# Optimization experiments

Measured on AMD Instinct MI355X. Metric: run time of the kernel, lower is better.

The kernel has to match this reference:

```python
import jax, jax.numpy as jnp
import numpy as np

B, S, H, NH = 2, 2048, 1024, 16
HD = H // NH  # 64
EPS = 1e-5


def setup_inputs() -> dict:
    key = jax.random.key(0)
    ks = jax.random.split(key, 4)
    return {
        "hidden_states": jax.random.normal(ks[0], (B, S, H), dtype=jnp.float32),
        "W_attn": jax.random.normal(ks[1], (H, 3 * H), dtype=jnp.float32) * (1.0 / np.sqrt(H)),
        "b_attn": jnp.zeros((3 * H,), dtype=jnp.float32),
        "W_proj": jax.random.normal(ks[2], (H, H), dtype=jnp.float32) * (1.0 / np.sqrt(H)),
        "b_proj": jnp.zeros((H,), dtype=jnp.float32),
        "q_gamma": jnp.ones((HD,), dtype=jnp.float32),
        "q_beta": jnp.zeros((HD,), dtype=jnp.float32),
        "k_gamma": jnp.ones((HD,), dtype=jnp.float32),
        "k_beta": jnp.zeros((HD,), dtype=jnp.float32),
    }


def _layernorm(x, gamma, beta):
    mu = jnp.mean(x, axis=-1, keepdims=True)
    var = jnp.mean(jnp.square(x - mu), axis=-1, keepdims=True)
    return (x - mu) * jax.lax.rsqrt(var + EPS) * gamma + beta


def reference(hidden_states, W_attn, b_attn, W_proj, b_proj, q_gamma, q_beta, k_gamma, k_beta):
    b, s, h = hidden_states.shape
    qkv = hidden_states @ W_attn + b_attn  # [B,S,3H]
    q, k, v = jnp.split(qkv, 3, axis=-1)
    # [B,S,H] -> [B,NH,S,HD]
    def to_heads(t):
        return t.reshape(b, s, NH, HD).transpose(0, 2, 1, 3)
    q, k, v = to_heads(q), to_heads(k), to_heads(v)
    # QK LayerNorm over head_dim
    q = _layernorm(q, q_gamma, q_beta)
    k = _layernorm(k, k_gamma, k_beta)
    scale = HD ** (-0.5)
    scores = jnp.einsum("bhqd,bhkd->bhqk", q, k) * scale
    causal = jnp.tril(jnp.ones((s, s), dtype=bool))
    mask_value = jnp.finfo(scores.dtype).min
    scores = jnp.where(causal, scores, mask_value)
    attn = jax.nn.softmax(scores.astype(jnp.float32), axis=-1).astype(q.dtype)
    out = jnp.einsum("bhqk,bhkd->bhqd", attn, v)
    out = out.transpose(0, 2, 1, 3).reshape(b, s, h)
    out = out @ W_proj + b_proj
    return out
```

## Files before the change

kernel.cpp:

```cpp
#include <hip/hip_runtime.h>
#include <hip/hip_bf16.h>

typedef __bf16 bf16x8 __attribute__((ext_vector_type(8)));
typedef float f32x4 __attribute__((ext_vector_type(4)));

#define EPS 1e-5f
#define QSCALE 0.18033688011112042f

__device__ __forceinline__ unsigned short f2bf(float f) {
  union { float f; unsigned int i; } c; c.f = f;
  unsigned int r = c.i + 0x7FFFu + ((c.i >> 16) & 1u);
  return (unsigned short)(r >> 16);
}

__global__ __launch_bounds__(256) void transpose_f32_bf16(
    const float* __restrict__ in, unsigned short* __restrict__ out,
    int R, int C)
{
  __shared__ __align__(16) unsigned short S[64 * 72];
  const int t = threadIdx.x;
  const int r = t >> 2, c4 = (t & 3) * 16;
  const int rt0 = blockIdx.y * 64, ct0 = blockIdx.x * 64;

  {
    long base = (long)(rt0 + r) * C + ct0 + c4;
    float4 a = *(const float4*)&in[base];
    float4 b = *(const float4*)&in[base + 4];
    float4 c = *(const float4*)&in[base + 8];
    float4 d = *(const float4*)&in[base + 12];
    unsigned short v[16] = {f2bf(a.x), f2bf(a.y), f2bf(a.z), f2bf(a.w),
                            f2bf(b.x), f2bf(b.y), f2bf(b.z), f2bf(b.w),
                            f2bf(c.x), f2bf(c.y), f2bf(c.z), f2bf(c.w),
                            f2bf(d.x), f2bf(d.y), f2bf(d.z), f2bf(d.w)};
    *(uint4*)&S[r * 72 + c4]     = *(uint4*)&v[0];
    *(uint4*)&S[r * 72 + c4 + 8] = *(uint4*)&v[8];
  }
  __syncthreads();

  unsigned short tmp[16];
#pragma unroll
  for (int j = 0; j < 16; j++) tmp[j] = S[(c4 + j) * 72 + r];
  *(uint4*)&out[(long)(ct0 + r) * R + rt0 + c4]     = *(uint4*)&tmp[0];
  *(uint4*)&out[(long)(ct0 + r) * R + rt0 + c4 + 8] = *(uint4*)&tmp[8];
}

__global__ __launch_bounds__(256) void convert_f32_bf16(
    const float* __restrict__ in, unsigned short* __restrict__ out)
{
  long i = ((long)blockIdx.x * 256 + threadIdx.x) * 16;
  float4 a = *(const float4*)&in[i];
  float4 b = *(const float4*)&in[i + 4];
  float4 c = *(const float4*)&in[i + 8];
  float4 d = *(const float4*)&in[i + 12];
  unsigned short v[16] = {f2bf(a.x), f2bf(a.y), f2bf(a.z), f2bf(a.w),
                          f2bf(b.x), f2bf(b.y), f2bf(b.z), f2bf(b.w),
                          f2bf(c.x), f2bf(c.y), f2bf(c.z), f2bf(c.w),
                          f2bf(d.x), f2bf(d.y), f2bf(d.z), f2bf(d.w)};
  *(uint4*)&out[i]     = *(uint4*)&v[0];
  *(uint4*)&out[i + 8] = *(uint4*)&v[8];
}

__global__ __launch_bounds__(256) void qkv_ln_kernel(
    const float* __restrict__ Xf,
    const unsigned short* __restrict__ Xbf, int use_xbf,
    const unsigned short* __restrict__ WT,
    const float* __restrict__ bias,
    const float* __restrict__ qg, const float* __restrict__ qb,
    const float* __restrict__ kg, const float* __restrict__ kb,
    unsigned short* __restrict__ Qws, unsigned short* __restrict__ Kws,
    unsigned short* __restrict__ Vws)
{
  __shared__ __align__(16) unsigned short As[2][128 * 32];
  __shared__ __align__(16) unsigned short Bs[2][128 * 32];

  const int tid = threadIdx.x;
  const int w = tid >> 6, lane = tid & 63, quad = lane >> 4, l15 = lane & 15;
  const int mh = w & 1, nh = w >> 1;
  const int n0 = blockIdx.x * 128, m0 = blockIdx.y * 128;

  f32x4 acc[4][4];
#pragma unroll
  for (int i = 0; i < 4; i++)
#pragma unroll
    for (int j = 0; j < 4; j++) acc[i][j] = (f32x4){0.f, 0.f, 0.f, 0.f};

  const int sr2 = tid >> 1, sh2 = (tid & 1) * 16;

  if (use_xbf) {
    long xo = (long)(m0 + sr2) * 1024 + sh2;
    *(uint4*)&As[0][sr2 * 32 + sh2]     = *(const uint4*)&Xbf[xo];
    *(uint4*)&As[0][sr2 * 32 + sh2 + 8] = *(const uint4*)&Xbf[xo + 8];
  } else {
    long xo = (long)(m0 + sr2) * 1024 + sh2;
    float4 a0 = *(const float4*)&Xf[xo];
    float4 a1 = *(const float4*)&Xf[xo + 4];
    float4 a2 = *(const float4*)&Xf[xo + 8];
    float4 a3 = *(const float4*)&Xf[xo + 12];
    unsigned short v[16] = {f2bf(a0.x), f2bf(a0.y), f2bf(a0.z), f2bf(a0.w),
                            f2bf(a1.x), f2bf(a1.y), f2bf(a1.z), f2bf(a1.w),
                            f2bf(a2.x), f2bf(a2.y), f2bf(a2.z), f2bf(a2.w),
                            f2bf(a3.x), f2bf(a3.y), f2bf(a3.z), f2bf(a3.w)};
    *(uint4*)&As[0][sr2 * 32 + sh2]     = *(uint4*)&v[0];
    *(uint4*)&As[0][sr2 * 32 + sh2 + 8] = *(uint4*)&v[8];
  }
  {
    long wo = (long)(n0 + sr2) * 1024 + sh2;
    *(uint4*)&Bs[0][sr2 * 32 + sh2]     = *(const uint4*)&WT[wo];
    *(uint4*)&Bs[0][sr2 * 32 + sh2 + 8] = *(const uint4*)&WT[wo + 8];
  }
  __syncthreads();

  int buf = 0;
  for (int kt = 0; kt < 1024; kt += 32) {
    const int nbuf = buf ^ 1;
    const bool pf = (kt + 32) < 1024;
    uint4 xv0, xv1, wv0, wv1;
    float4 a0, a1, a2, a3;
    if (pf) {
      if (use_xbf) {
        long xo = (long)(m0 + sr2) * 1024 + kt + 32 + sh2;
        xv0 = *(const uint4*)&Xbf[xo];
        xv1 = *(const uint4*)&Xbf[xo + 8];
      } else {
        long xo = (long)(m0 + sr2) * 1024 + kt + 32 + sh2;
        a0 = *(const float4*)&Xf[xo];
        a1 = *(const float4*)&Xf[xo + 4];
        a2 = *(const float4*)&Xf[xo + 8];
        a3 = *(const float4*)&Xf[xo + 12];
      }
      long wo = (long)(n0 + sr2) * 1024 + kt + 32 + sh2;
      wv0 = *(const uint4*)&WT[wo];
      wv1 = *(const uint4*)&WT[wo + 8];
    }

    bf16x8 af[4], bfr[4];
#pragma unroll
    for (int mq = 0; mq < 4; mq++)
      af[mq] = *(const bf16x8*)&As[buf][(mh * 64 + mq * 16 + l15) * 32 + quad * 8];
#pragma unroll
    for (int nq = 0; nq < 4; nq++)
      bfr[nq] = *(const bf16x8*)&Bs[buf][(nh * 64 + nq * 16 + l15) * 32 + quad * 8];
#pragma unroll
    for (int mq = 0; mq < 4; mq++)
#pragma unroll
      for (int nq = 0; nq < 4; nq++)
        acc[mq][nq] = __builtin_amdgcn_mfma_f32_16x16x32_bf16(af[mq], bfr[nq], acc[mq][nq], 0, 0, 0);

    if (pf) {
      if (use_xbf) {
        *(uint4*)&As[nbuf][sr2 * 32 + sh2]     = xv0;
        *(uint4*)&As[nbuf][sr2 * 32 + sh2 + 8] = xv1;
      } else {
        unsigned short v[16] = {f2bf(a0.x), f2bf(a0.y), f2bf(a0.z), f2bf(a0.w),
                                f2bf(a1.x), f2bf(a1.y), f2bf(a1.z), f2bf(a1.w),
                                f2bf(a2.x), f2bf(a2.y), f2bf(a2.z), f2bf(a2.w),
                                f2bf(a3.x), f2bf(a3.y), f2bf(a3.z), f2bf(a3.w)};
        *(uint4*)&As[nbuf][sr2 * 32 + sh2]     = *(uint4*)&v[0];
        *(uint4*)&As[nbuf][sr2 * 32 + sh2 + 8] = *(uint4*)&v[8];
      }
      *(uint4*)&Bs[nbuf][sr2 * 32 + sh2]     = wv0;
      *(uint4*)&Bs[nbuf][sr2 * 32 + sh2 + 8] = wv1;
    }
    __syncthreads();
    buf = nbuf;
  }

#pragma unroll
  for (int nq = 0; nq < 4; nq++) {
    float bv = bias[n0 + nh * 64 + nq * 16 + l15];
#pragma unroll
    for (int mq = 0; mq < 4; mq++)
#pragma unroll
      for (int rr = 0; rr < 4; rr++) acc[mq][nq][rr] += bv;
  }

  const int g = (n0 >> 6) + nh;
  const bool isQ = g < 16, isK = (g >= 16) && (g < 32);

  if (isQ || isK) {
    float gv[4], bev[4];
#pragma unroll
    for (int nq = 0; nq < 4; nq++) {
      int d = nq * 16 + l15;
      gv[nq]  = isQ ? qg[d] : kg[d];
      bev[nq] = isQ ? qb[d] : kb[d];
      if (isQ) { gv[nq] *= QSCALE; bev[nq] *= QSCALE; }
    }
#pragma unroll
    for (int mq = 0; mq < 4; mq++)
#pragma unroll
      for (int rr = 0; rr < 4; rr++) {
        float s  = acc[mq][0][rr] + acc[mq][1][rr] + acc[mq][2][rr] + acc[mq][3][rr];
        float s2 = acc[mq][0][rr]*acc[mq][0][rr] + acc[mq][1][rr]*acc[mq][1][rr]
                 + acc[mq][2][rr]*acc[mq][2][rr] + acc[mq][3][rr]*acc[mq][3][rr];
#pragma unroll
        for (int off = 1; off < 16; off <<= 1) {
          s  += __shfl_xor(s,  off, 64);
          s2 += __shfl_xor(s2, off, 64);
        }
        float mu   = s * (1.0f / 64.0f);
        float var  = fmaxf(s2 * (1.0f / 64.0f) - mu * mu, 0.f);
        float rstd = rsqrtf(var + EPS);
#pragma unroll
        for (int nq = 0; nq < 4; nq++)
          acc[mq][nq][rr] = (acc[mq][nq][rr] - mu) * rstd * gv[nq] + bev[nq];
      }
  }

  unsigned short* dst; int head;
  if (isQ)      { dst = Qws; head = g; }
  else if (isK) { dst = Kws; head = g - 16; }
  else          { dst = Vws; head = g - 32; }

#pragma unroll
  for (int mq = 0; mq < 4; mq++)
#pragma unroll
    for (int rr = 0; rr < 4; rr++) {
      int m = m0 + mh * 64 + mq * 16 + quad * 4 + rr;
      int b = m >> 11, s = m & 2047;
      long base = ((long)((b * 16 + head) * 2048 + s)) * 64;
#pragma unroll
      for (int nq = 0; nq < 4; nq++)
        dst[base + nq * 16 + l15] = f2bf(acc[mq][nq][rr]);
    }
}

__global__ __launch_bounds__(256) void attn_kernel(
    unsigned short* __restrict__ Qws,
    const unsigned short* __restrict__ Kws,
    const unsigned short* __restrict__ Vws)
{
  __shared__ __align__(16) unsigned short Ks[2][64 * 72];
  __shared__ __align__(16) unsigned short VTs[2][64 * 72];
  __shared__ __align__(16) unsigned short Ps[64 * 64];

  const int tid = threadIdx.x;
  const int w = tid >> 6, lane = tid & 63, quad = lane >> 4, l15 = lane & 15;
  const int bh = blockIdx.y;
  const int qt = ((bh >> 3) & 1) ? blockIdx.x : (31 - blockIdx.x);
  const int qbase = qt * 64;
  const long bhoff = (long)bh * 2048 * 64;
  const int jmax = qt + 1;

  const int sr = tid >> 2, sc = (tid & 3) * 16;
  const int vrow = lane, vc = w * 16;

  *(uint4*)&Ps[sr * 64 + sc]     = *(const uint4*)&Qws[bhoff + (qbase + sr) * 64 + sc];
  *(uint4*)&Ps[sr * 64 + sc + 8] = *(const uint4*)&Qws[bhoff + (qbase + sr) * 64 + sc + 8];
  *(uint4*)&Ks[0][sr * 72 + sc]     = *(const uint4*)&Kws[bhoff + sr * 64 + sc];
  *(uint4*)&Ks[0][sr * 72 + sc + 8] = *(const uint4*)&Kws[bhoff + sr * 64 + sc + 8];
  {
    uint4 v0 = *(const uint4*)&Vws[bhoff + vrow * 64 + vc];
    uint4 v1 = *(const uint4*)&Vws[bhoff + vrow * 64 + vc + 8];
    const unsigned short* vv = (const unsigned short*)&v0;
#pragma unroll
    for (int t = 0; t < 8; t++) VTs[0][(vc + t) * 72 + vrow] = vv[t];
    vv = (const unsigned short*)&v1;
#pragma unroll
    for (int t = 0; t < 8; t++) VTs[0][(vc + 8 + t) * 72 + vrow] = vv[t];
  }
  __syncthreads();

  const bf16x8 qf0 = *(const bf16x8*)&Ps[(w * 16 + l15) * 64 + quad * 8];
  const bf16x8 qf1 = *(const bf16x8*)&Ps[(w * 16 + l15) * 64 + 32 + quad * 8];
  __syncthreads();

  bf16x8 ones;
  {
    union { unsigned short u[8]; bf16x8 v; } c;
#pragma unroll
    for (int i = 0; i < 8; i++) c.u[i] = 0x3F80u;
    ones = c.v;
  }

  f32x4 o[4], osum;
#pragma unroll
  for (int i = 0; i < 4; i++) o[i] = (f32x4){0.f, 0.f, 0.f, 0.f};
  osum = (f32x4){0.f, 0.f, 0.f, 0.f};

  const int sw = ((l15 >> 2) & 3) << 4;
  const int pc0 = (quad * 8) ^ sw;
  const int pc1 = (32 + quad * 8) ^ sw;

  int buf = 0;
  for (int j = 0; j < jmax; j++) {
    const int nbuf = buf ^ 1;
    const int kb = j * 64;
    const bool pf = (j + 1) < jmax;
    uint4 pk0, pk1, pv0, pv1;
    if (pf) {
      const int kb1 = kb + 64;
      pk0 = *(const uint4*)&Kws[bhoff + (kb1 + sr) * 64 + sc];
      pk1 = *(const uint4*)&Kws[bhoff + (kb1 + sr) * 64 + sc + 8];
      pv0 = *(const uint4*)&Vws[bhoff + (kb1 + vrow) * 64 + vc];
      pv1 = *(const uint4*)&Vws[bhoff + (kb1 + vrow) * 64 + vc + 8];
    }

    f32x4 sacc[4];
#pragma unroll
    for (int i = 0; i < 4; i++) sacc[i] = (f32x4){0.f, 0.f, 0.f, 0.f};
#pragma unroll
    for (int nt = 0; nt < 4; nt++) {
      bf16x8 kf0 = *(const bf16x8*)&Ks[buf][(nt * 16 + l15) * 72 + quad * 8];
      bf16x8 kf1 = *(const bf16x8*)&Ks[buf][(nt * 16 + l15) * 72 + 32 + quad * 8];
      sacc[nt] = __builtin_amdgcn_mfma_f32_16x16x32_bf16(qf0, kf0, sacc[nt], 0, 0, 0);
      sacc[nt] = __builtin_amdgcn_mfma_f32_16x16x32_bf16(qf1, kf1, sacc[nt], 0, 0, 0);
    }

    if (pf) {
      *(uint4*)&Ks[nbuf][sr * 72 + sc]     = pk0;
      *(uint4*)&Ks[nbuf][sr * 72 + sc + 8] = pk1;
      const unsigned short* vv = (const unsigned short*)&pv0;
#pragma unroll
      for (int t = 0; t < 8; t++) VTs[nbuf][(vc + t) * 72 + vrow] = vv[t];
      vv = (const unsigned short*)&pv1;
#pragma unroll
      for (int t = 0; t < 8; t++) VTs[nbuf][(vc + 8 + t) * 72 + vrow] = vv[t];
    }

    const bool domask = (j == qt);
#pragma unroll
    for (int nt = 0; nt < 4; nt++)
#pragma unroll
      for (int rr = 0; rr < 4; rr++) {
        float p = exp2f(sacc[nt][rr]);
        if (domask) {
          int kcol = kb + nt * 16 + l15;
          int qrow = qbase + w * 16 + quad * 4 + rr;
          if (kcol > qrow) p = 0.f;
        }
        sacc[nt][rr] = p;
      }

#pragma unroll
    for (int rr = 0; rr < 4; rr++)
#pragma unroll
      for (int nt = 0; nt < 4; nt++)
        Ps[(w * 16 + quad * 4 + rr) * 64 + (((nt ^ quad) & 3) * 16 + l15)]
            = f2bf(sacc[nt][rr]);

    bf16x8 pfr0 = *(const bf16x8*)&Ps[(w * 16 + l15) * 64 + pc0];
    bf16x8 pfr1 = *(const bf16x8*)&Ps[(w * 16 + l15) * 64 + pc1];

    osum = __builtin_amdgcn_mfma_f32_16x16x32_bf16(pfr0, ones, osum, 0, 0, 0);
    osum = __builtin_amdgcn_mfma_f32_16x16x32_bf16(pfr1, ones, osum, 0, 0, 0);
#pragma unroll
    for (int dt = 0; dt < 4; dt++) {
      bf16x8 vf0 = *(const bf16x8*)&VTs[buf][(dt * 16 + l15) * 72 + quad * 8];
      bf16x8 vf1 = *(const bf16x8*)&VTs[buf][(dt * 16 + l15) * 72 + 32 + quad * 8];
      o[dt] = __builtin_amdgcn_mfma_f32_16x16x32_bf16(pfr0, vf0, o[dt], 0, 0, 0);
      o[dt] = __builtin_amdgcn_mfma_f32_16x16x32_bf16(pfr1, vf1, o[dt], 0, 0, 0);
    }
    __syncthreads();
    buf = nbuf;
  }

#pragma unroll
  for (int rr = 0; rr < 4; rr++) {
    float inv = 1.0f / osum[rr];
    int row = qbase + w * 16 + quad * 4 + rr;
    long base = bhoff + (long)row * 64;
#pragma unroll
    for (int dt = 0; dt < 4; dt++)
      Qws[base + dt * 16 + l15] = f2bf(o[dt][rr] * inv);
  }
}

__global__ __launch_bounds__(256) void proj_kernel(
    const unsigned short* __restrict__ AQ,
    const unsigned short* __restrict__ WT,
    const float* __restrict__ bias,
    float* __restrict__ Out)
{
  __shared__ __align__(16) unsigned short As[2][128 * 32];
  __shared__ __align__(16) unsigned short Bs[2][128 * 32];

  const int tid = threadIdx.x;
  const int w = tid >> 6, lane = tid & 63, quad = lane >> 4, l15 = lane & 15;
  const int mh = w & 1, nh = w >> 1;
  const int n0 = blockIdx.x * 128, m0 = blockIdx.y * 128;

  f32x4 acc[4][4];
#pragma unroll
  for (int i = 0; i < 4; i++)
#pragma unroll
    for (int j = 0; j < 4; j++) acc[i][j] = (f32x4){0.f, 0.f, 0.f, 0.f};

  const int sr2 = tid >> 1, sh2 = (tid & 1) * 16;
  const int m = m0 + sr2, b = m >> 11, s = m & 2047;

  {
    const int h = sh2 >> 6, d = sh2 & 63;
    long ao = ((long)((b * 16 + h) * 2048 + s)) * 64 + d;
    *(uint4*)&As[0][sr2 * 32 + sh2]     = *(const uint4*)&AQ[ao];
    *(uint4*)&As[0][sr2 * 32 + sh2 + 8] = *(const uint4*)&AQ[ao + 8];
    long wo = (long)(n0 + sr2) * 1024 + sh2;
    *(uint4*)&Bs[0][sr2 * 32 + sh2]     = *(const uint4*)&WT[wo];
    *(uint4*)&Bs[0][sr2 * 32 + sh2 + 8] = *(const uint4*)&WT[wo + 8];
  }
  __syncthreads();

  int buf = 0;
  for (int kt = 0; kt < 1024; kt += 32) {
    const int nbuf = buf ^ 1;
    const bool pf = (kt + 32) < 1024;
    uint4 av0, av1, wv0, wv1;
    if (pf) {
      const int k = kt + 32 + sh2, h = k >> 6, d = k & 63;
      long ao = ((long)((b * 16 + h) * 2048 + s)) * 64 + d;
      av0 = *(const uint4*)&AQ[ao];
      av1 = *(const uint4*)&AQ[ao + 8];
      long wo = (long)(n0 + sr2) * 1024 + kt + 32 + sh2;
      wv0 = *(const uint4*)&WT[wo];
      wv1 = *(const uint4*)&WT[wo + 8];
    }

    bf16x8 af[4], bfr[4];
#pragma unroll
    for (int mq = 0; mq < 4; mq++)
      af[mq] = *(const bf16x8*)&As[buf][(mh * 64 + mq * 16 + l15) * 32 + quad * 8];
#pragma unroll
    for (int nq = 0; nq < 4; nq++)
      bfr[nq] = *(const bf16x8*)&Bs[buf][(nh * 64 + nq * 16 + l15) * 32 + quad * 8];
#pragma unroll
    for (int mq = 0; mq < 4; mq++)
#pragma unroll
      for (int nq = 0; nq < 4; nq++)
        acc[mq][nq] = __builtin_amdgcn_mfma_f32_16x16x32_bf16(af[mq], bfr[nq], acc[mq][nq], 0, 0, 0);

    if (pf) {
      *(uint4*)&As[nbuf][sr2 * 32 + sh2]     = av0;
      *(uint4*)&As[nbuf][sr2 * 32 + sh2 + 8] = av1;
      *(uint4*)&Bs[nbuf][sr2 * 32 + sh2]     = wv0;
      *(uint4*)&Bs[nbuf][sr2 * 32 + sh2 + 8] = wv1;
    }
    __syncthreads();
    buf = nbuf;
  }

#pragma unroll
  for (int nq = 0; nq < 4; nq++) {
    int n = n0 + nh * 64 + nq * 16 + l15;
    float bv = bias[n];
#pragma unroll
    for (int mq = 0; mq < 4; mq++)
#pragma unroll
      for (int rr = 0; rr < 4; rr++) {
        int mm = m0 + mh * 64 + mq * 16 + quad * 4 + rr;
        Out[(long)mm * 1024 + n] = acc[mq][nq][rr] + bv;
      }
  }
}

extern "C" void kernel_launch(void* const* d_in, const int* in_sizes, int n_in,
                              void* d_out, int out_size, void* d_ws, size_t ws_size,
                              hipStream_t stream) {
  const float* X  = (const float*)d_in[0];
  const float* Wa = (const float*)d_in[1];
  const float* ba = (const float*)d_in[2];
  const float* Wp = (const float*)d_in[3];
  const float* bp = (const float*)d_in[4];
  const float* qg = (const float*)d_in[5];
  const float* qb = (const float*)d_in[6];
  const float* kg = (const float*)d_in[7];
  const float* kb = (const float*)d_in[8];

  const long per = 2L * 16 * 2048 * 64;
  unsigned short* ws  = (unsigned short*)d_ws;
  unsigned short* Qws = ws;
  unsigned short* Kws = Qws + per;
  unsigned short* Vws = Kws + per;

  const bool big = ws_size >= (size_t)(5L * per * 2);
  unsigned short *Xbf, *WaT, *WpT;
  if (big) {
    Xbf = Vws + per;
    WaT = Xbf + per;
    WpT = WaT + 3072L * 1024;
  } else {
    Xbf = Qws;
    WaT = Vws + per;
    WpT = WaT + 3072L * 1024;
  }

  transpose_f32_bf16<<<dim3(48, 16), 256, 0, stream>>>(Wa, WaT, 1024, 3072);
  transpose_f32_bf16<<<dim3(16, 16), 256, 0, stream>>>(Wp, WpT, 1024, 1024);
  if (big) convert_f32_bf16<<<1024, 256, 0, stream>>>(X, Xbf);
  qkv_ln_kernel<<<dim3(24, 32), 256, 0, stream>>>(X, Xbf, big ? 1 : 0, WaT, ba,
                                                  qg, qb, kg, kb, Qws, Kws, Vws);
  attn_kernel<<<dim3(32, 32), 256, 0, stream>>>(Qws, Kws, Vws);
  proj_kernel<<<dim3(8, 32), 256, 0, stream>>>(Qws, WpT, bp, (float*)d_out);
}
```

Before: 243.4 us.

## Compute V directly in transposed layout via separate GEMM kernel; single-buffer attention LDS

Moves the V projection out of the QKV kernel into a new GEMM, W_v^T times X^T, that writes V already transposed per head ([B,NH,HD,S]). The attention kernel can then load V^T tiles with vector copies instead of scattering 16 scalar LDS writes per thread. The attention K and V^T shared buffers are cut from double to single buffering, with an extra barrier pair around each refill. Launch bounds are raised to ask for 6 blocks per CU, trading load/compute overlap inside a block for occupancy. This adds a kernel launch, and the V GEMM writes scattered 2-byte stores along S.

After: 222.1 us. 1.1x faster.

```diff
diff --git a/kernel.cpp b/kernel.cpp
--- a/kernel.cpp
+++ b/kernel.cpp
@@ -67,8 +67,7 @@
     const float* __restrict__ bias,
     const float* __restrict__ qg, const float* __restrict__ qb,
     const float* __restrict__ kg, const float* __restrict__ kb,
-    unsigned short* __restrict__ Qws, unsigned short* __restrict__ Kws,
-    unsigned short* __restrict__ Vws)
+    unsigned short* __restrict__ Qws, unsigned short* __restrict__ Kws)
 {
   __shared__ __align__(16) unsigned short As[2][128 * 32];
   __shared__ __align__(16) unsigned short Bs[2][128 * 32];
@@ -175,9 +174,9 @@
   }
 
   const int g = (n0 >> 6) + nh;
-  const bool isQ = g < 16, isK = (g >= 16) && (g < 32);
-
-  if (isQ || isK) {
+  const bool isQ = g < 16;
+
+  {
     float gv[4], bev[4];
 #pragma unroll
     for (int nq = 0; nq < 4; nq++) {
@@ -207,10 +206,8 @@
       }
   }
 
-  unsigned short* dst; int head;
-  if (isQ)      { dst = Qws; head = g; }
-  else if (isK) { dst = Kws; head = g - 16; }
-  else          { dst = Vws; head = g - 32; }
+  unsigned short* dst = isQ ? Qws : Kws;
+  const int head = isQ ? g : g - 16;
 
 #pragma unroll
   for (int mq = 0; mq < 4; mq++)
@@ -225,13 +222,130 @@
     }
 }
 
-__global__ __launch_bounds__(256) void attn_kernel(
+__global__ __launch_bounds__(256) void vt_kernel(
+    const float* __restrict__ Xf,
+    const unsigned short* __restrict__ Xbf, int use_xbf,
+    const unsigned short* __restrict__ WvT,
+    const float* __restrict__ bias,
+    unsigned short* __restrict__ Vt)
+{
+  __shared__ __align__(16) unsigned short As[2][128 * 32];
+  __shared__ __align__(16) unsigned short Bs[2][128 * 32];
+
+  const int tid = threadIdx.x;
+  const int w = tid >> 6, lane = tid & 63, quad = lane >> 4, l15 = lane & 15;
+  const int mh = w & 1, nh = w >> 1;
+  const int n0 = blockIdx.x * 128, m0 = blockIdx.y * 128, bz = blockIdx.z;
+  const long xrow0 = (long)bz * 2048;
+
+  f32x4 acc[4][4];
+#pragma unroll
+  for (int i = 0; i < 4; i++)
+#pragma unroll
+    for (int j = 0; j < 4; j++) acc[i][j] = (f32x4){0.f, 0.f, 0.f, 0.f};
+
+  const int sr2 = tid >> 1, sh2 = (tid & 1) * 16;
+
+  {
+    long wo = (long)(m0 + sr2) * 1024 + sh2;
+    *(uint4*)&As[0][sr2 * 32 + sh2]     = *(const uint4*)&WvT[wo];
+    *(uint4*)&As[0][sr2 * 32 + sh2 + 8] = *(const uint4*)&WvT[wo + 8];
+  }
+  if (use_xbf) {
+    long xo = (xrow0 + n0 + sr2) * 1024 + sh2;
+    *(uint4*)&Bs[0][sr2 * 32 + sh2]     = *(const uint4*)&Xbf[xo];
+    *(uint4*)&Bs[0][sr2 * 32 + sh2 + 8] = *(const uint4*)&Xbf[xo + 8];
+  } else {
+    long xo = (xrow0 + n0 + sr2) * 1024 + sh2;
+    float4 a0 = *(const float4*)&Xf[xo];
+    float4 a1 = *(const float4*)&Xf[xo + 4];
+    float4 a2 = *(const float4*)&Xf[xo + 8];
+    float4 a3 = *(const float4*)&Xf[xo + 12];
+    unsigned short v[16] = {f2bf(a0.x), f2bf(a0.y), f2bf(a0.z), f2bf(a0.w),
+                            f2bf(a1.x), f2bf(a1.y), f2bf(a1.z), f2bf(a1.w),
+                            f2bf(a2.x), f2bf(a2.y), f2bf(a2.z), f2bf(a2.w),
+                            f2bf(a3.x), f2bf(a3.y), f2bf(a3.z), f2bf(a3.w)};
+    *(uint4*)&Bs[0][sr2 * 32 + sh2]     = *(uint4*)&v[0];
+    *(uint4*)&Bs[0][sr2 * 32 + sh2 + 8] = *(uint4*)&v[8];
+  }
+  __syncthreads();
+
+  int buf = 0;
+  for (int kt = 0; kt < 1024; kt += 32) {
+    const int nbuf = buf ^ 1;
+    const bool pf = (kt + 32) < 1024;
+    uint4 wv0, wv1, xv0, xv1;
+    float4 a0, a1, a2, a3;
+    if (pf) {
+      long wo = (long)(m0 + sr2) * 1024 + kt + 32 + sh2;
+      wv0 = *(const uint4*)&WvT[wo];
+      wv1 = *(const uint4*)&WvT[wo + 8];
+      long xo = (xrow0 + n0 + sr2) * 1024 + kt + 32 + sh2;
+      if (use_xbf) {
+        xv0 = *(const uint4*)&Xbf[xo];
+        xv1 = *(const uint4*)&Xbf[xo + 8];
+      } else {
+        a0 = *(const float4*)&Xf[xo];
+        a1 = *(const float4*)&Xf[xo + 4];
+        a2 = *(const float4*)&Xf[xo + 8];
+        a3 = *(const float4*)&Xf[xo + 12];
+      }
+    }
+
+    bf16x8 af[4], bfr[4];
+#pragma unroll
+    for (int mq = 0; mq < 4; mq++)
+      af[mq] = *(const bf16x8*)&As[buf][(mh * 64 + mq * 16 + l15) * 32 + quad * 8];
+#pragma unroll
+    for (int nq = 0; nq < 4; nq++)
+      bfr[nq] = *(const bf16x8*)&Bs[buf][(nh * 64 + nq * 16 + l15) * 32 + quad * 8];
+#pragma unroll
+    for (int mq = 0; mq < 4; mq++)
+#pragma unroll
+      for (int nq = 0; nq < 4; nq++)
+        acc[mq][nq] = __builtin_amdgcn_mfma_f32_16x16x32_bf16(af[mq], bfr[nq], acc[mq][nq], 0, 0, 0);
+
+    if (pf) {
+      *(uint4*)&As[nbuf][sr2 * 32 + sh2]     = wv0;
+      *(uint4*)&As[nbuf][sr2 * 32 + sh2 + 8] = wv1;
+      if (use_xbf) {
+        *(uint4*)&Bs[nbuf][sr2 * 32 + sh2]     = xv0;
+        *(uint4*)&Bs[nbuf][sr2 * 32 + sh2 + 8] = xv1;
+      } else {
+        unsigned short v[16] = {f2bf(a0.x), f2bf(a0.y), f2bf(a0.z), f2bf(a0.w),
+                                f2bf(a1.x), f2bf(a1.y), f2bf(a1.z), f2bf(a1.w),
+                                f2bf(a2.x), f2bf(a2.y), f2bf(a2.z), f2bf(a2.w),
+                                f2bf(a3.x), f2bf(a3.y), f2bf(a3.z), f2bf(a3.w)};
+        *(uint4*)&Bs[nbuf][sr2 * 32 + sh2]     = *(uint4*)&v[0];
+        *(uint4*)&Bs[nbuf][sr2 * 32 + sh2 + 8] = *(uint4*)&v[8];
+      }
+    }
+    __syncthreads();
+    buf = nbuf;
+  }
+
+  const long outb = (long)bz * 2097152;
+#pragma unroll
+  for (int mq = 0; mq < 4; mq++)
+#pragma unroll
+    for (int rr = 0; rr < 4; rr++) {
+      int m = m0 + mh * 64 + mq * 16 + quad * 4 + rr;
+      float bv = bias[2048 + m];
+#pragma unroll
+      for (int nq = 0; nq < 4; nq++) {
+        int n = n0 + nh * 64 + nq * 16 + l15;
+        Vt[outb + (long)m * 2048 + n] = f2bf(acc[mq][nq][rr] + bv);
+      }
+    }
+}
+
+__global__ __launch_bounds__(256, 6) void attn_kernel(
     unsigned short* __restrict__ Qws,
     const unsigned short* __restrict__ Kws,
-    const unsigned short* __restrict__ Vws)
+    const unsigned short* __restrict__ Vt)
 {
-  __shared__ __align__(16) unsigned short Ks[2][64 * 72];
-  __shared__ __align__(16) unsigned short VTs[2][64 * 72];
+  __shared__ __align__(16) unsigned short Ks[64 * 72];
+  __shared__ __align__(16) unsigned short VTs[64 * 72];
   __shared__ __align__(16) unsigned short Ps[64 * 64];
 
   const int tid = threadIdx.x;
@@ -240,30 +354,21 @@
   const int qt = ((bh >> 3) & 1) ? blockIdx.x : (31 - blockIdx.x);
   const int qbase = qt * 64;
   const long bhoff = (long)bh * 2048 * 64;
+  const long bhv   = (long)bh * 131072;
   const int jmax = qt + 1;
 
   const int sr = tid >> 2, sc = (tid & 3) * 16;
-  const int vrow = lane, vc = w * 16;
 
   *(uint4*)&Ps[sr * 64 + sc]     = *(const uint4*)&Qws[bhoff + (qbase + sr) * 64 + sc];
   *(uint4*)&Ps[sr * 64 + sc + 8] = *(const uint4*)&Qws[bhoff + (qbase + sr) * 64 + sc + 8];
-  *(uint4*)&Ks[0][sr * 72 + sc]     = *(const uint4*)&Kws[bhoff + sr * 64 + sc];
-  *(uint4*)&Ks[0][sr * 72 + sc + 8] = *(const uint4*)&Kws[bhoff + sr * 64 + sc + 8];
-  {
-    uint4 v0 = *(const uint4*)&Vws[bhoff + vrow * 64 + vc];
-    uint4 v1 = *(const uint4*)&Vws[bhoff + vrow * 64 + vc + 8];
-    const unsigned short* vv = (const unsigned short*)&v0;
-#pragma unroll
-    for (int t = 0; t < 8; t++) VTs[0][(vc + t) * 72 + vrow] = vv[t];
-    vv = (const unsigned short*)&v1;
-#pragma unroll
-    for (int t = 0; t < 8; t++) VTs[0][(vc + 8 + t) * 72 + vrow] = vv[t];
-  }
+  *(uint4*)&Ks[sr * 72 + sc]      = *(const uint4*)&Kws[bhoff + sr * 64 + sc];
+  *(uint4*)&Ks[sr * 72 + sc + 8]  = *(const uint4*)&Kws[bhoff + sr * 64 + sc + 8];
+  *(uint4*)&VTs[sr * 72 + sc]     = *(const uint4*)&Vt[bhv + sr * 2048 + sc];
+  *(uint4*)&VTs[sr * 72 + sc + 8] = *(const uint4*)&Vt[bhv + sr * 2048 + sc + 8];
   __syncthreads();
 
   const bf16x8 qf0 = *(const bf16x8*)&Ps[(w * 16 + l15) * 64 + quad * 8];
   const bf16x8 qf1 = *(const bf16x8*)&Ps[(w * 16 + l15) * 64 + 32 + quad * 8];
-  __syncthreads();
 
   bf16x8 ones;
   {
@@ -282,9 +387,7 @@
   const int pc0 = (quad * 8) ^ sw;
   const int pc1 = (32 + quad * 8) ^ sw;
 
-  int buf = 0;
   for (int j = 0; j < jmax; j++) {
-    const int nbuf = buf ^ 1;
     const int kb = j * 64;
     const bool pf = (j + 1) < jmax;
     uint4 pk0, pk1, pv0, pv1;
@@ -292,8 +395,8 @@
       const int kb1 = kb + 64;
       pk0 = *(const uint4*)&Kws[bhoff + (kb1 + sr) * 64 + sc];
       pk1 = *(const uint4*)&Kws[bhoff + (kb1 + sr) * 64 + sc + 8];
-      pv0 = *(const uint4*)&Vws[bhoff + (kb1 + vrow) * 64 + vc];
-      pv1 = *(const uint4*)&Vws[bhoff + (kb1 + vrow) * 64 + vc + 8];
+      pv0 = *(const uint4*)&Vt[bhv + sr * 2048 + kb1 + sc];
+      pv1 = *(const uint4*)&Vt[bhv + sr * 2048 + kb1 + sc + 8];
     }
 
     f32x4 sacc[4];
@@ -301,21 +404,10 @@
     for (int i = 0; i < 4; i++) sacc[i] = (f32x4){0.f, 0.f, 0.f, 0.f};
 #pragma unroll
     for (int nt = 0; nt < 4; nt++) {
-      bf16x8 kf0 = *(const bf16x8*)&Ks[buf][(nt * 16 + l15) * 72 + quad * 8];
-      bf16x8 kf1 = *(const bf16x8*)&Ks[buf][(nt * 16 + l15) * 72 + 32 + quad * 8];
+      bf16x8 kf0 = *(const bf16x8*)&Ks[(nt * 16 + l15) * 72 + quad * 8];
+      bf16x8 kf1 = *(const bf16x8*)&Ks[(nt * 16 + l15) * 72 + 32 + quad * 8];
       sacc[nt] = __builtin_amdgcn_mfma_f32_16x16x32_bf16(qf0, kf0, sacc[nt], 0, 0, 0);
       sacc[nt] = __builtin_amdgcn_mfma_f32_16x16x32_bf16(qf1, kf1, sacc[nt], 0, 0, 0);
-    }
-
-    if (pf) {
-      *(uint4*)&Ks[nbuf][sr * 72 + sc]     = pk0;
-      *(uint4*)&Ks[nbuf][sr * 72 + sc + 8] = pk1;
-      const unsigned short* vv = (const unsigned short*)&pv0;
-#pragma unroll
-      for (int t = 0; t < 8; t++) VTs[nbuf][(vc + t) * 72 + vrow] = vv[t];
-      vv = (const unsigned short*)&pv1;
-#pragma unroll
-      for (int t = 0; t < 8; t++) VTs[nbuf][(vc + 8 + t) * 72 + vrow] = vv[t];
     }
 
     const bool domask = (j == qt);
@@ -346,13 +438,20 @@
     osum = __builtin_amdgcn_mfma_f32_16x16x32_bf16(pfr1, ones, osum, 0, 0, 0);
 #pragma unroll
     for (int dt = 0; dt < 4; dt++) {
-      bf16x8 vf0 = *(const bf16x8*)&VTs[buf][(dt * 16 + l15) * 72 + quad * 8];
-      bf16x8 vf1 = *(const bf16x8*)&VTs[buf][(dt * 16 + l15) * 72 + 32 + quad * 8];
+      bf16x8 vf0 = *(const bf16x8*)&VTs[(dt * 16 + l15) * 72 + quad * 8];
+      bf16x8 vf1 = *(const bf16x8*)&VTs[(dt * 16 + l15) * 72 + 32 + quad * 8];
       o[dt] = __builtin_amdgcn_mfma_f32_16x16x32_bf16(pfr0, vf0, o[dt], 0, 0, 0);
       o[dt] = __builtin_amdgcn_mfma_f32_16x16x32_bf16(pfr1, vf1, o[dt], 0, 0, 0);
     }
-    __syncthreads();
-    buf = nbuf;
+
+    if (pf) {
+      __syncthreads();
+      *(uint4*)&Ks[sr * 72 + sc]      = pk0;
+      *(uint4*)&Ks[sr * 72 + sc + 8]  = pk1;
+      *(uint4*)&VTs[sr * 72 + sc]     = pv0;
+      *(uint4*)&VTs[sr * 72 + sc + 8] = pv1;
+      __syncthreads();
+    }
   }
 
 #pragma unroll
@@ -469,25 +568,27 @@
   unsigned short* ws  = (unsigned short*)d_ws;
   unsigned short* Qws = ws;
   unsigned short* Kws = Qws + per;
-  unsigned short* Vws = Kws + per;
+  unsigned short* Vt  = Kws + per;
 
   const bool big = ws_size >= (size_t)(5L * per * 2);
   unsigned short *Xbf, *WaT, *WpT;
   if (big) {
-    Xbf = Vws + per;
+    Xbf = Vt + per;
     WaT = Xbf + per;
     WpT = WaT + 3072L * 1024;
   } else {
     Xbf = Qws;
-    WaT = Vws + per;
+    WaT = Vt + per;
     WpT = WaT + 3072L * 1024;
   }
+  unsigned short* WvT = WaT + 2048L * 1024;
 
   transpose_f32_bf16<<<dim3(48, 16), 256, 0, stream>>>(Wa, WaT, 1024, 3072);
   transpose_f32_bf16<<<dim3(16, 16), 256, 0, stream>>>(Wp, WpT, 1024, 1024);
   if (big) convert_f32_bf16<<<1024, 256, 0, stream>>>(X, Xbf);
-  qkv_ln_kernel<<<dim3(24, 32), 256, 0, stream>>>(X, Xbf, big ? 1 : 0, WaT, ba,
-                                                  qg, qb, kg, kb, Qws, Kws, Vws);
-  attn_kernel<<<dim3(32, 32), 256, 0, stream>>>(Qws, Kws, Vws);
+  qkv_ln_kernel<<<dim3(16, 32), 256, 0, stream>>>(X, Xbf, big ? 1 : 0, WaT, ba,
+                                                  qg, qb, kg, kb, Qws, Kws);
+  vt_kernel<<<dim3(16, 8, 2), 256, 0, stream>>>(X, Xbf, big ? 1 : 0, WvT, ba, Vt);
+  attn_kernel<<<dim3(32, 32), 256, 0, stream>>>(Qws, Kws, Vt);
   proj_kernel<<<dim3(8, 32), 256, 0, stream>>>(Qws, WpT, bp, (float*)d_out);
 }
```
